# Performance work log

Measured on AMD Instinct MI355X. Metric: run time of the kernel, lower is better.

The kernel has to match this reference:

```python
import jax, jax.numpy as jnp
import numpy as np
from jax import lax

DIM = 256
NUM_HEADS = 8
HEAD_DIM = DIM // NUM_HEADS
DN = ('NCHW', 'OIHW', 'NCHW')


def _dsconv(x, dw, dwb, pw, pwb):
    # depthwise 3x3 (groups = C) then pointwise 1x1
    C = x.shape[1]
    y = lax.conv_general_dilated(x, dw, (1, 1), 'SAME',
                                 dimension_numbers=DN,
                                 feature_group_count=C)
    y = y + dwb[None, :, None, None]
    y = lax.conv_general_dilated(y, pw, (1, 1), 'SAME', dimension_numbers=DN)
    return y + pwb[None, :, None, None]


def _to_heads(x):
    # (B, C, H, W) -> (B, nh, HW, hd)
    B, C, H, W = x.shape
    return x.reshape(B, NUM_HEADS, HEAD_DIM, H * W).transpose(0, 1, 3, 2)


def setup_inputs() -> dict:
    key = jax.random.key(0)
    ks = jax.random.split(key, 14)
    B, H, W = 2, 64, 64
    inp = {
        'x': jax.random.normal(ks[0], (B, DIM, H, W), jnp.float32),
        'ctx': jax.random.normal(ks[1], (B, DIM, H, W), jnp.float32),
    }
    i = 2
    for name in ('q', 'k', 'v'):
        inp[f'{name}_dw'] = jax.random.normal(ks[i], (DIM, 1, 3, 3), jnp.float32) * 0.05; i += 1
        inp[f'{name}_dwb'] = jnp.zeros((DIM,), jnp.float32)
        inp[f'{name}_pw'] = jax.random.normal(ks[i], (DIM, DIM, 1, 1), jnp.float32) * 0.05; i += 1
        inp[f'{name}_pwb'] = jnp.zeros((DIM,), jnp.float32)
    return inp


def reference(x, ctx,
              q_dw, q_dwb, q_pw, q_pwb,
              k_dw, k_dwb, k_pw, k_pwb,
              v_dw, v_dwb, v_pw, v_pwb):
    B, C, H, W = x.shape
    scale = HEAD_DIM ** 0.5
    q = _to_heads(_dsconv(x, q_dw, q_dwb, q_pw, q_pwb))    # (B, nh, HW, hd)
    k = _to_heads(_dsconv(ctx, k_dw, k_dwb, k_pw, k_pwb))
    v = _to_heads(_dsconv(ctx, v_dw, v_dwb, v_pw, v_pwb))
    attn = jnp.einsum('bnqd,bnkd->bnqk', q, k) / scale      # (B, nh, HW, HW)
    attn = jax.nn.softmax(attn, axis=-1)
    out = jnp.einsum('bnqk,bnkd->bnqd', attn, v)            # (B, nh, HW, hd)
    out = out.transpose(0, 1, 3, 2).reshape(B, DIM, H * W)  # (B, dim, HW)
    return out
```

## Files before the change

### kernel.cpp

```cpp
#include <hip/hip_runtime.h>
#include <hip/hip_bf16.h>


#define HW 4096
#define CDIM 256
#define SCALE_LOG2E 0.2550348543f

typedef short bf16x8 __attribute__((ext_vector_type(8)));
typedef float f32x2 __attribute__((ext_vector_type(2)));
typedef float f32x4 __attribute__((ext_vector_type(4)));
typedef float f32x16 __attribute__((ext_vector_type(16)));

__device__ inline unsigned short f2bf(float f) {
  unsigned u = __float_as_uint(f);
  u = (u + 0x7fffu + ((u >> 16) & 1u)) >> 16;
  return (unsigned short)u;
}

__device__ inline unsigned cvtpk(float lo, float hi) {
  unsigned r;
  asm("v_cvt_pk_bf16_f32 %0, %1, %2" : "=v"(r) : "v"(lo), "v"(hi));
  return r;
}

__device__ inline float fexp2(float x) {
#if __has_builtin(__builtin_amdgcn_exp2f)
  return __builtin_amdgcn_exp2f(x);
#else
  return exp2f(x);
#endif
}

__device__ inline void plswap(unsigned& a, unsigned& b) {
#if __has_builtin(__builtin_amdgcn_permlane32_swap)
  auto r = __builtin_amdgcn_permlane32_swap((int)a, (int)b, false, false);
  a = (unsigned)r[0];
  b = (unsigned)r[1];
#else
  unsigned as = __shfl_xor((int)a, 32), bs = __shfl_xor((int)b, 32);
  bool hi = (threadIdx.x & 32) != 0;
  unsigned na = hi ? bs : a;
  unsigned nb = hi ? b : as;
  a = na; b = nb;
#endif
}

__global__ __launch_bounds__(256) void dw_all(
    const float* __restrict__ x, const float* __restrict__ ctx,
    const float* __restrict__ qdw, const float* __restrict__ qdwb,
    const float* __restrict__ kdw, const float* __restrict__ kdwb,
    const float* __restrict__ vdw, const float* __restrict__ vdwb,
    unsigned short* __restrict__ tq, unsigned short* __restrict__ tk,
    unsigned short* __restrict__ tv) {
  int gid = blockIdx.x * 256 + threadIdx.x;
  int pass = gid >> 19;
  int r = gid & 524287;
  int q4 = r & 1023;
  int plane = r >> 10;
  int c = plane & 255;
  int w0 = (q4 & 15) * 4, h = q4 >> 4;
  const float* src = (pass ? ctx : x) + (size_t)plane * HW;

  float e[3][6];
#pragma unroll
  for (int kh = 0; kh < 3; ++kh) {
    int hh = h + kh - 1;
    if (hh < 0 || hh > 63) {
#pragma unroll
      for (int j = 0; j < 6; ++j) e[kh][j] = 0.f;
    } else {
      const float* row = src + hh * 64 + w0;
      float4 m = *(const float4*)row;
      e[kh][0] = (w0 > 0) ? row[-1] : 0.f;
      e[kh][1] = m.x; e[kh][2] = m.y; e[kh][3] = m.z; e[kh][4] = m.w;
      e[kh][5] = (w0 < 60) ? row[4] : 0.f;
    }
  }
  size_t obase = (size_t)plane * HW + h * 64 + w0;
  if (pass == 0) {
    const float* wc = qdw + c * 9;
    float bv = qdwb[c];
    float a0 = bv, a1 = bv, a2 = bv, a3 = bv;
#pragma unroll
    for (int kh = 0; kh < 3; ++kh) {
      float w_0 = wc[kh * 3], w_1 = wc[kh * 3 + 1], w_2 = wc[kh * 3 + 2];
      a0 += w_0 * e[kh][0] + w_1 * e[kh][1] + w_2 * e[kh][2];
      a1 += w_0 * e[kh][1] + w_1 * e[kh][2] + w_2 * e[kh][3];
      a2 += w_0 * e[kh][2] + w_1 * e[kh][3] + w_2 * e[kh][4];
      a3 += w_0 * e[kh][3] + w_1 * e[kh][4] + w_2 * e[kh][5];
    }
    *(ushort4*)(tq + obase) = make_ushort4(f2bf(a0), f2bf(a1), f2bf(a2), f2bf(a3));
  } else {
    const float* wk = kdw + c * 9;
    const float* wvv = vdw + c * 9;
    float bk = kdwb[c], bv2 = vdwb[c];
    float k0 = bk, k1 = bk, k2 = bk, k3 = bk;
    float v0 = bv2, v1 = bv2, v2 = bv2, v3 = bv2;
#pragma unroll
    for (int kh = 0; kh < 3; ++kh) {
      float kw0 = wk[kh * 3], kw1 = wk[kh * 3 + 1], kw2 = wk[kh * 3 + 2];
      float vw0 = wvv[kh * 3], vw1 = wvv[kh * 3 + 1], vw2 = wvv[kh * 3 + 2];
      k0 += kw0 * e[kh][0] + kw1 * e[kh][1] + kw2 * e[kh][2];
      k1 += kw0 * e[kh][1] + kw1 * e[kh][2] + kw2 * e[kh][3];
      k2 += kw0 * e[kh][2] + kw1 * e[kh][3] + kw2 * e[kh][4];
      k3 += kw0 * e[kh][3] + kw1 * e[kh][4] + kw2 * e[kh][5];
      v0 += vw0 * e[kh][0] + vw1 * e[kh][1] + vw2 * e[kh][2];
      v1 += vw0 * e[kh][1] + vw1 * e[kh][2] + vw2 * e[kh][3];
      v2 += vw0 * e[kh][2] + vw1 * e[kh][3] + vw2 * e[kh][4];
      v3 += vw0 * e[kh][3] + vw1 * e[kh][4] + vw2 * e[kh][5];
    }
    *(ushort4*)(tk + obase) = make_ushort4(f2bf(k0), f2bf(k1), f2bf(k2), f2bf(k3));
    *(ushort4*)(tv + obase) = make_ushort4(f2bf(v0), f2bf(v1), f2bf(v2), f2bf(v3));
  }
}

__global__ __launch_bounds__(256) void pw_all(
    const unsigned short* __restrict__ tq, const unsigned short* __restrict__ tk,
    const unsigned short* __restrict__ tv,
    const float* __restrict__ qw, const float* __restrict__ qbs,
    const float* __restrict__ kw, const float* __restrict__ kbs,
    const float* __restrict__ vw, const float* __restrict__ vbs,
    unsigned short* __restrict__ Qc, unsigned short* __restrict__ Kc,
    unsigned short* __restrict__ Vc) {
  __shared__ __align__(16) unsigned char Bs[64 * 512];
  int tt = blockIdx.x >> 9;
  int bid = blockIdx.x & 511;
  const unsigned short* t = tt == 0 ? tq : (tt == 1 ? tk : tv);
  const float* w = tt == 0 ? qw : (tt == 1 ? kw : vw);
  const float* bias = tt == 0 ? qbs : (tt == 1 ? kbs : vbs);
  unsigned short* out = tt == 0 ? Qc : (tt == 1 ? Kc : Vc);
  float oscale = tt == 0 ? SCALE_LOG2E : 1.0f;

  int pt = bid & 63, cot = (bid >> 6) & 3, bb = bid >> 8;
  int p0 = pt * 64, co0 = cot * 64;
  int tid = threadIdx.x;
  int wv = tid >> 6, l = tid & 63, lq = l & 15, lg = l >> 4;

  bf16x8 af[8];
  {
    const float* wr = w + (size_t)(co0 + wv * 16 + lq) * 256;
#pragma unroll
    for (int kt = 0; kt < 8; ++kt) {
      float4 a = *(const float4*)(wr + kt * 32 + lg * 8);
      float4 bq = *(const float4*)(wr + kt * 32 + lg * 8 + 4);
      union { unsigned u[4]; bf16x8 v; } cv;
      cv.u[0] = cvtpk(a.x, a.y);  cv.u[1] = cvtpk(a.z, a.w);
      cv.u[2] = cvtpk(bq.x, bq.y); cv.u[3] = cvtpk(bq.z, bq.w);
      af[kt] = cv.v;
    }
  }
  {
    int cb = tid >> 3, po = tid & 7;
    const unsigned short* src = t + (size_t)bb * (CDIM * HW) + (size_t)(cb * 8) * HW + p0 + po * 8;
    uint4 r[8];
#pragma unroll
    for (int i = 0; i < 8; ++i) r[i] = *(const uint4*)(src + (size_t)i * HW);
#pragma unroll
    for (int jj = 0; jj < 8; ++jj) {
      uint4 o;
#pragma unroll
      for (int ww = 0; ww < 4; ++ww) {
        unsigned a = ((const unsigned*)&r[2 * ww])[jj >> 1];
        unsigned b = ((const unsigned*)&r[2 * ww + 1])[jj >> 1];
        unsigned lo = (jj & 1) ? (a >> 16) : (a & 0xffffu);
        unsigned hi = (jj & 1) ? (b & 0xffff0000u) : (b << 16);
        (&o.x)[ww] = lo | hi;
      }
      int p = po * 8 + jj;
      int swz = ((p ^ (p >> 3)) & 7) << 4;
      *(uint4*)(Bs + p * 512 + ((cb * 16) ^ swz)) = o;
    }
  }
  __syncthreads();
  f32x4 acc[4] = {};
#pragma unroll
  for (int nt = 0; nt < 4; ++nt) {
    int p = nt * 16 + lq;
    int swz = ((p ^ (p >> 3)) & 7) << 4;
    const unsigned char* Bp = Bs + p * 512;
#pragma unroll
    for (int kt = 0; kt < 8; ++kt) {
      bf16x8 bf = *(const bf16x8*)(Bp + ((kt * 64 + lg * 16) ^ swz));
      acc[nt] = __builtin_amdgcn_mfma_f32_16x16x32_bf16(af[kt], bf, acc[nt], 0, 0, 0);
    }
  }
  if (tt < 2) {
    int co = co0 + wv * 16 + lg * 4;
    int d0 = co & 31;
    float b0 = bias[co], b1 = bias[co + 1], b2 = bias[co + 2], b3 = bias[co + 3];
    size_t rowb = (size_t)(bb * 8 + (co >> 5)) * HW;
#pragma unroll
    for (int nt = 0; nt < 4; ++nt) {
      int p = p0 + nt * 16 + lq;
      ushort4 pk = make_ushort4(f2bf((acc[nt][0] + b0) * oscale),
                                f2bf((acc[nt][1] + b1) * oscale),
                                f2bf((acc[nt][2] + b2) * oscale),
                                f2bf((acc[nt][3] + b3) * oscale));
      *(ushort4*)(out + (rowb + p) * 32 + d0) = pk;
    }
  } else {
    int cob = co0 + wv * 16 + lg * 4;
#pragma unroll
    for (int r = 0; r < 4; ++r) {
      float bv = bias[cob + r];
      size_t rb = (size_t)bb * (CDIM * HW) + (size_t)(cob + r) * HW + p0;
#pragma unroll
      for (int nt = 0; nt < 4; ++nt)
        out[rb + nt * 16 + lq] = f2bf(acc[nt][r] + bv);
    }
  }
}

struct AttnState {
  bf16x8 qfh0, qfh1;
  f32x16 OA, OB, ZZ;
  float ps;
  int lq, hi;
};

__device__ inline void attn_compute(AttnState& S, const unsigned char* Kcur,
                                    const unsigned char* Vcur) {
#pragma unroll
  for (int t2 = 0; t2 < 2; ++t2) {
    const unsigned char* Krow = Kcur + (t2 * 32 + S.lq) * 80 + S.hi * 16;
    bf16x8 kfa = *(const bf16x8*)(Krow);
    bf16x8 kfb = *(const bf16x8*)(Krow + 32);
    __builtin_amdgcn_s_setprio(1);
    f32x16 st = __builtin_amdgcn_mfma_f32_32x32x16_bf16(kfa, S.qfh0, S.ZZ, 0, 0, 0);
    st = __builtin_amdgcn_mfma_f32_32x32x16_bf16(kfb, S.qfh1, st, 0, 0, 0);
    __builtin_amdgcn_s_setprio(0);
    float p[16];
#pragma unroll
    for (int r = 0; r < 16; ++r) p[r] = fexp2(st[r]);
    f32x2 a0 = {p[0], p[1]},  a1 = {p[2], p[3]};
    f32x2 a2 = {p[4], p[5]},  a3 = {p[6], p[7]};
    f32x2 a4 = {p[8], p[9]},  a5 = {p[10], p[11]};
    f32x2 a6 = {p[12], p[13]}, a7 = {p[14], p[15]};
    f32x2 b0 = a0 + a1, b1 = a2 + a3, b2 = a4 + a5, b3 = a6 + a7;
    f32x2 c0 = b0 + b1, c1 = b2 + b3;
    f32x2 d0 = c0 + c1;
    S.ps += d0[0] + d0[1];
    unsigned u0 = cvtpk(p[0], p[1]),  u1 = cvtpk(p[2], p[3]);
    unsigned u2 = cvtpk(p[4], p[5]),  u3 = cvtpk(p[6], p[7]);
    unsigned u4 = cvtpk(p[8], p[9]),  u5 = cvtpk(p[10], p[11]);
    unsigned u6 = cvtpk(p[12], p[13]), u7 = cvtpk(p[14], p[15]);
    plswap(u0, u2);
    plswap(u1, u3);
    plswap(u4, u6);
    plswap(u5, u7);
    union { unsigned w[4]; bf16x8 v; } A0, A1;
    A0.w[0] = u0; A0.w[1] = u1; A0.w[2] = u2; A0.w[3] = u3;
    A1.w[0] = u4; A1.w[1] = u5; A1.w[2] = u6; A1.w[3] = u7;
    const unsigned char* Vrow = Vcur + S.lq * 144 + t2 * 64;
    bf16x8 vf0 = *(const bf16x8*)(Vrow + S.hi * 16);
    bf16x8 vf1 = *(const bf16x8*)(Vrow + 32 + S.hi * 16);
    __builtin_amdgcn_s_setprio(1);
    S.OA = __builtin_amdgcn_mfma_f32_32x32x16_bf16(A0.v, vf0, S.OA, 0, 0, 0);
    S.OB = __builtin_amdgcn_mfma_f32_32x32x16_bf16(A1.v, vf1, S.OB, 0, 0, 0);
    __builtin_amdgcn_s_setprio(0);
  }
}

__global__ __launch_bounds__(512, 4) void attn_kernel(
    const unsigned short* __restrict__ Qt, const unsigned short* __restrict__ Kt,
    const unsigned short* __restrict__ Vn, float* __restrict__ out) {
  __shared__ __align__(16) unsigned char lds[38912];
  int bid0 = blockIdx.x;
  int bid = (bid0 & 7) * 64 + (bid0 >> 3);
  int qb = bid & 31, bh = bid >> 5;
  int b = bh >> 3, n = bh & 7;
  int tid = threadIdx.x;
  int l = tid & 63, wv = tid >> 6;
  int qg = wv & 3, ks = wv >> 2;

  AttnState S;
  S.lq = l & 31; S.hi = l >> 5;
  S.OA = (f32x16){}; S.OB = (f32x16){}; S.ZZ = (f32x16){};
  S.ps = 0.f;

  const unsigned short* Qg = Qt + (size_t)bh * (HW * 32);
  const unsigned short* Kg = Kt + (size_t)bh * (HW * 32);
  const unsigned short* Vg = Vn + (size_t)(b * CDIM + n * 32) * HW;

  int q0 = qb * 128 + qg * 32;
  S.qfh0 = *(const bf16x8*)(Qg + (size_t)(q0 + S.lq) * 32 + S.hi * 8);
  S.qfh1 = *(const bf16x8*)(Qg + (size_t)(q0 + S.lq) * 32 + 16 + S.hi * 8);

  int ht = tid & 255;
  int krow = ht >> 2, kcol = ht & 3;
  int vrow = ht >> 3, vcol = ht & 7;
  unsigned char* Kb0 = lds + (ks * 2 + 0) * 5120;
  unsigned char* Kb1 = lds + (ks * 2 + 1) * 5120;
  unsigned char* Vb0 = lds + 20480 + (ks * 2 + 0) * 4608;
  unsigned char* Vb1 = lds + 20480 + (ks * 2 + 1) * 4608;
  unsigned char* Kw0 = Kb0 + krow * 80 + kcol * 16;
  unsigned char* Kw1 = Kb1 + krow * 80 + kcol * 16;
  unsigned char* Vw0 = Vb0 + vrow * 144 + vcol * 16;
  unsigned char* Vw1 = Vb1 + vrow * 144 + vcol * 16;
  const uint4* Ksrc = (const uint4*)(Kg + (size_t)(ks * 2048) * 32);
  const unsigned short* Vsrc = Vg + (size_t)vrow * HW + ks * 2048 + vcol * 8;

  uint4 kst = Ksrc[krow * 4 + kcol];
  uint4 vst = *(const uint4*)Vsrc;
  *(uint4*)Kw0 = kst;
  *(uint4*)Vw0 = vst;
  kst = Ksrc[(64 + krow) * 4 + kcol];
  vst = *(const uint4*)(Vsrc + 64);

#pragma unroll 1
  for (int c = 0; c < 32; c += 2) {
    __syncthreads();
    *(uint4*)Kw1 = kst;
    *(uint4*)Vw1 = vst;
    if (c < 30) {
      kst = Ksrc[((c + 2) * 64 + krow) * 4 + kcol];
      vst = *(const uint4*)(Vsrc + (c + 2) * 64);
    }
    attn_compute(S, Kb0, Vb0);
    __syncthreads();
    if (c < 30) {
      *(uint4*)Kw0 = kst;
      *(uint4*)Vw0 = vst;
      kst = Ksrc[((c + 3) * 64 + krow) * 4 + kcol];
      vst = *(const uint4*)(Vsrc + (c + 3) * 64);
    }
    attn_compute(S, Kb1, Vb1);
  }

  f32x16 O = S.OA + S.OB;
  float ps = S.ps;
  int lq = S.lq, hi = S.hi;
  ps += __shfl_xor(ps, 32);
  __syncthreads();
  float* Ox = (float*)lds;
  float* SumX = (float*)(lds + 16896);
  if (ks == 1) {
    float* Or = Ox + qg * (32 * 33) + lq * 33;
#pragma unroll
    for (int rr = 0; rr < 4; ++rr) {
      float4 vv = {O[rr * 4 + 0], O[rr * 4 + 1], O[rr * 4 + 2], O[rr * 4 + 3]};
      *(float4*)(Or + 8 * rr + 4 * hi) = vv;
    }
    if (hi == 0) SumX[qg * 32 + lq] = ps;
  }
  __syncthreads();
  if (ks == 0) {
    const float* Or = Ox + qg * (32 * 33) + lq * 33;
    float rtot = ps + SumX[qg * 32 + lq];
    float rv = 1.0f / rtot;
    size_t ob = ((size_t)(b * CDIM) + n * 32 + lq) * HW;
#pragma unroll
    for (int rr = 0; rr < 4; ++rr) {
      int qlb = 8 * rr + 4 * hi;
      float4 part = *(const float4*)(Or + qlb);
      float4 res;
#pragma unroll
      for (int j = 0; j < 4; ++j) {
        float sq = __int_as_float(
            __builtin_amdgcn_ds_bpermute((qlb + j) * 4, __float_as_int(rv)));
        (&res.x)[j] = (O[rr * 4 + j] + (&part.x)[j]) * sq;
      }
      *(float4*)(out + ob + q0 + qlb) = res;
    }
  }
}

extern "C" void kernel_launch(void* const* d_in, const int* in_sizes, int n_in,
                              void* d_out, int out_size, void* d_ws, size_t ws_size,
                              hipStream_t stream) {
  const float* x   = (const float*)d_in[0];
  const float* ctx = (const float*)d_in[1];
  const float* q_dw  = (const float*)d_in[2];
  const float* q_dwb = (const float*)d_in[3];
  const float* q_pw  = (const float*)d_in[4];
  const float* q_pwb = (const float*)d_in[5];
  const float* k_dw  = (const float*)d_in[6];
  const float* k_dwb = (const float*)d_in[7];
  const float* k_pw  = (const float*)d_in[8];
  const float* k_pwb = (const float*)d_in[9];
  const float* v_dw  = (const float*)d_in[10];
  const float* v_dwb = (const float*)d_in[11];
  const float* v_pw  = (const float*)d_in[12];
  const float* v_pwb = (const float*)d_in[13];

  const size_t N = (size_t)2 * CDIM * HW;
  unsigned short* Qc = (unsigned short*)d_ws;
  unsigned short* Kc = Qc + N;
  unsigned short* Vc = Kc + N;
  unsigned short* tv = Vc + N;
  unsigned short* tq = (unsigned short*)d_out;
  unsigned short* tk = tq + N;

  dw_all<<<4096, 256, 0, stream>>>(x, ctx, q_dw, q_dwb, k_dw, k_dwb, v_dw, v_dwb,
                                   tq, tk, tv);
  pw_all<<<1536, 256, 0, stream>>>(tq, tk, tv, q_pw, q_pwb, k_pw, k_pwb,
                                   v_pw, v_pwb, Qc, Kc, Vc);
  attn_kernel<<<512, 512, 0, stream>>>(Qc, Kc, Vc, (float*)d_out);
}
```

Measured before the change: 85.61 us.

## Process two query tiles per wave and split keys four ways in 1024-thread blocks

Each wave now holds two 32-row query tiles and reuses every K/V fragment read from LDS for both, which halves LDS fragment traffic per unit of work. Blocks grow to 1024 threads with four key splits, so there are 256 blocks of 256 queries each. A multi-stage LDS reduction merges the four partial outputs and row sums. The cost is higher register pressure, a larger LDS footprint that limits resident blocks, and fewer blocks than CUs, which may leave some hardware idle.

Result: slower. 141.2 us (+64.9%).

```diff
diff --git a/kernel.cpp b/kernel.cpp
--- a/kernel.cpp
+++ b/kernel.cpp
@@ -211,156 +211,221 @@
   }
 }
 
-struct AttnState {
-  bf16x8 qfh0, qfh1;
-  f32x16 OA, OB, ZZ;
-  float ps;
+
+__device__ inline void softmax_tile(const f32x16& st, float& ps, bf16x8& A0v, bf16x8& A1v) {
+  float p[16];
+#pragma unroll
+  for (int r = 0; r < 16; ++r) p[r] = fexp2(st[r]);
+  f32x2 a0 = {p[0], p[1]},  a1 = {p[2], p[3]};
+  f32x2 a2 = {p[4], p[5]},  a3 = {p[6], p[7]};
+  f32x2 a4 = {p[8], p[9]},  a5 = {p[10], p[11]};
+  f32x2 a6 = {p[12], p[13]}, a7 = {p[14], p[15]};
+  f32x2 b0 = a0 + a1, b1 = a2 + a3, b2 = a4 + a5, b3 = a6 + a7;
+  f32x2 c0 = b0 + b1, c1 = b2 + b3;
+  f32x2 d0 = c0 + c1;
+  ps += d0[0] + d0[1];
+  unsigned u0 = cvtpk(p[0], p[1]),  u1 = cvtpk(p[2], p[3]);
+  unsigned u2 = cvtpk(p[4], p[5]),  u3 = cvtpk(p[6], p[7]);
+  unsigned u4 = cvtpk(p[8], p[9]),  u5 = cvtpk(p[10], p[11]);
+  unsigned u6 = cvtpk(p[12], p[13]), u7 = cvtpk(p[14], p[15]);
+  plswap(u0, u2);
+  plswap(u1, u3);
+  plswap(u4, u6);
+  plswap(u5, u7);
+  union { unsigned w[4]; bf16x8 v; } A0, A1;
+  A0.w[0] = u0; A0.w[1] = u1; A0.w[2] = u2; A0.w[3] = u3;
+  A1.w[0] = u4; A1.w[1] = u5; A1.w[2] = u6; A1.w[3] = u7;
+  A0v = A0.v; A1v = A1.v;
+}
+
+struct AState {
+  bf16x8 qa0, qa1, qb0, qb1;
+  f32x16 Oa, Ob, ZZ;
+  float psa, psb;
   int lq, hi;
 };
 
-__device__ inline void attn_compute(AttnState& S, const unsigned char* Kcur,
-                                    const unsigned char* Vcur) {
+__device__ inline void attn_compute(AState& S, const unsigned char* Kb,
+                                    const unsigned char* Vb) {
 #pragma unroll
   for (int t2 = 0; t2 < 2; ++t2) {
-    const unsigned char* Krow = Kcur + (t2 * 32 + S.lq) * 80 + S.hi * 16;
+    const unsigned char* Krow = Kb + (t2 * 32 + S.lq) * 80 + S.hi * 16;
     bf16x8 kfa = *(const bf16x8*)(Krow);
     bf16x8 kfb = *(const bf16x8*)(Krow + 32);
-    __builtin_amdgcn_s_setprio(1);
-    f32x16 st = __builtin_amdgcn_mfma_f32_32x32x16_bf16(kfa, S.qfh0, S.ZZ, 0, 0, 0);
-    st = __builtin_amdgcn_mfma_f32_32x32x16_bf16(kfb, S.qfh1, st, 0, 0, 0);
-    __builtin_amdgcn_s_setprio(0);
-    float p[16];
-#pragma unroll
-    for (int r = 0; r < 16; ++r) p[r] = fexp2(st[r]);
-    f32x2 a0 = {p[0], p[1]},  a1 = {p[2], p[3]};
-    f32x2 a2 = {p[4], p[5]},  a3 = {p[6], p[7]};
-    f32x2 a4 = {p[8], p[9]},  a5 = {p[10], p[11]};
-    f32x2 a6 = {p[12], p[13]}, a7 = {p[14], p[15]};
-    f32x2 b0 = a0 + a1, b1 = a2 + a3, b2 = a4 + a5, b3 = a6 + a7;
-    f32x2 c0 = b0 + b1, c1 = b2 + b3;
-    f32x2 d0 = c0 + c1;
-    S.ps += d0[0] + d0[1];
-    unsigned u0 = cvtpk(p[0], p[1]),  u1 = cvtpk(p[2], p[3]);
-    unsigned u2 = cvtpk(p[4], p[5]),  u3 = cvtpk(p[6], p[7]);
-    unsigned u4 = cvtpk(p[8], p[9]),  u5 = cvtpk(p[10], p[11]);
-    unsigned u6 = cvtpk(p[12], p[13]), u7 = cvtpk(p[14], p[15]);
-    plswap(u0, u2);
-    plswap(u1, u3);
-    plswap(u4, u6);
-    plswap(u5, u7);
-    union { unsigned w[4]; bf16x8 v; } A0, A1;
-    A0.w[0] = u0; A0.w[1] = u1; A0.w[2] = u2; A0.w[3] = u3;
-    A1.w[0] = u4; A1.w[1] = u5; A1.w[2] = u6; A1.w[3] = u7;
-    const unsigned char* Vrow = Vcur + S.lq * 144 + t2 * 64;
+    const unsigned char* Vrow = Vb + S.lq * 176 + t2 * 64;
     bf16x8 vf0 = *(const bf16x8*)(Vrow + S.hi * 16);
     bf16x8 vf1 = *(const bf16x8*)(Vrow + 32 + S.hi * 16);
     __builtin_amdgcn_s_setprio(1);
-    S.OA = __builtin_amdgcn_mfma_f32_32x32x16_bf16(A0.v, vf0, S.OA, 0, 0, 0);
-    S.OB = __builtin_amdgcn_mfma_f32_32x32x16_bf16(A1.v, vf1, S.OB, 0, 0, 0);
+    f32x16 st = __builtin_amdgcn_mfma_f32_32x32x16_bf16(kfa, S.qa0, S.ZZ, 0, 0, 0);
+    st = __builtin_amdgcn_mfma_f32_32x32x16_bf16(kfb, S.qa1, st, 0, 0, 0);
     __builtin_amdgcn_s_setprio(0);
-  }
-}
-
-__global__ __launch_bounds__(512, 4) void attn_kernel(
+    bf16x8 A0, A1;
+    softmax_tile(st, S.psa, A0, A1);
+    __builtin_amdgcn_s_setprio(1);
+    S.Oa = __builtin_amdgcn_mfma_f32_32x32x16_bf16(A0, vf0, S.Oa, 0, 0, 0);
+    S.Oa = __builtin_amdgcn_mfma_f32_32x32x16_bf16(A1, vf1, S.Oa, 0, 0, 0);
+    st = __builtin_amdgcn_mfma_f32_32x32x16_bf16(kfa, S.qb0, S.ZZ, 0, 0, 0);
+    st = __builtin_amdgcn_mfma_f32_32x32x16_bf16(kfb, S.qb1, st, 0, 0, 0);
+    __builtin_amdgcn_s_setprio(0);
+    softmax_tile(st, S.psb, A0, A1);
+    __builtin_amdgcn_s_setprio(1);
+    S.Ob = __builtin_amdgcn_mfma_f32_32x32x16_bf16(A0, vf0, S.Ob, 0, 0, 0);
+    S.Ob = __builtin_amdgcn_mfma_f32_32x32x16_bf16(A1, vf1, S.Ob, 0, 0, 0);
+    __builtin_amdgcn_s_setprio(0);
+  }
+}
+
+__global__ __launch_bounds__(1024, 4) void attn_kernel(
     const unsigned short* __restrict__ Qt, const unsigned short* __restrict__ Kt,
     const unsigned short* __restrict__ Vn, float* __restrict__ out) {
-  __shared__ __align__(16) unsigned char lds[38912];
+  __shared__ __align__(16) unsigned char lds[86016];
   int bid0 = blockIdx.x;
-  int bid = (bid0 & 7) * 64 + (bid0 >> 3);
-  int qb = bid & 31, bh = bid >> 5;
+  int bid = (bid0 & 7) * 32 + (bid0 >> 3);
+  int qb = bid & 15, bh = bid >> 4;
   int b = bh >> 3, n = bh & 7;
   int tid = threadIdx.x;
   int l = tid & 63, wv = tid >> 6;
   int qg = wv & 3, ks = wv >> 2;
 
-  AttnState S;
+  AState S;
   S.lq = l & 31; S.hi = l >> 5;
-  S.OA = (f32x16){}; S.OB = (f32x16){}; S.ZZ = (f32x16){};
-  S.ps = 0.f;
+  S.Oa = (f32x16){}; S.Ob = (f32x16){}; S.ZZ = (f32x16){};
+  S.psa = 0.f; S.psb = 0.f;
 
   const unsigned short* Qg = Qt + (size_t)bh * (HW * 32);
   const unsigned short* Kg = Kt + (size_t)bh * (HW * 32);
   const unsigned short* Vg = Vn + (size_t)(b * CDIM + n * 32) * HW;
 
-  int q0 = qb * 128 + qg * 32;
-  S.qfh0 = *(const bf16x8*)(Qg + (size_t)(q0 + S.lq) * 32 + S.hi * 8);
-  S.qfh1 = *(const bf16x8*)(Qg + (size_t)(q0 + S.lq) * 32 + 16 + S.hi * 8);
-
-  int ht = tid & 255;
-  int krow = ht >> 2, kcol = ht & 3;
-  int vrow = ht >> 3, vcol = ht & 7;
-  unsigned char* Kb0 = lds + (ks * 2 + 0) * 5120;
-  unsigned char* Kb1 = lds + (ks * 2 + 1) * 5120;
-  unsigned char* Vb0 = lds + 20480 + (ks * 2 + 0) * 4608;
-  unsigned char* Vb1 = lds + 20480 + (ks * 2 + 1) * 4608;
-  unsigned char* Kw0 = Kb0 + krow * 80 + kcol * 16;
-  unsigned char* Kw1 = Kb1 + krow * 80 + kcol * 16;
-  unsigned char* Vw0 = Vb0 + vrow * 144 + vcol * 16;
-  unsigned char* Vw1 = Vb1 + vrow * 144 + vcol * 16;
-  const uint4* Ksrc = (const uint4*)(Kg + (size_t)(ks * 2048) * 32);
-  const unsigned short* Vsrc = Vg + (size_t)vrow * HW + ks * 2048 + vcol * 8;
-
-  uint4 kst = Ksrc[krow * 4 + kcol];
-  uint4 vst = *(const uint4*)Vsrc;
+  int q0 = qb * 256 + qg * 64;
+  S.qa0 = *(const bf16x8*)(Qg + (size_t)(q0 + S.lq) * 32 + S.hi * 8);
+  S.qa1 = *(const bf16x8*)(Qg + (size_t)(q0 + S.lq) * 32 + 16 + S.hi * 8);
+  S.qb0 = *(const bf16x8*)(Qg + (size_t)(q0 + 32 + S.lq) * 32 + S.hi * 8);
+  S.qb1 = *(const bf16x8*)(Qg + (size_t)(q0 + 32 + S.lq) * 32 + 16 + S.hi * 8);
+
+  int sk = tid >> 8, r = tid & 255;
+  int krow = r >> 2, kcol = r & 3;
+  int vrow = r >> 3, vcol = r & 7;
+  unsigned char* Kp0 = lds + sk * 10240;
+  unsigned char* Vp0 = lds + 40960 + sk * 11264;
+  unsigned char* Kw0 = Kp0 + krow * 80 + kcol * 16;
+  unsigned char* Kw1 = Kw0 + 5120;
+  unsigned char* Vw0 = Vp0 + vrow * 176 + vcol * 16;
+  unsigned char* Vw1 = Vw0 + 5632;
+  const uint4* Ksrc4 = (const uint4*)(Kg + (size_t)(sk * 1024) * 32);
+  const unsigned short* Vsrcp = Vg + (size_t)vrow * HW + sk * 1024 + vcol * 8;
+
+  const unsigned char* Kb0 = lds + ks * 10240;
+  const unsigned char* Kb1 = Kb0 + 5120;
+  const unsigned char* Vb0 = lds + 40960 + ks * 11264;
+  const unsigned char* Vb1 = Vb0 + 5632;
+
+  uint4 kst = Ksrc4[krow * 4 + kcol];
+  uint4 vst = *(const uint4*)Vsrcp;
   *(uint4*)Kw0 = kst;
   *(uint4*)Vw0 = vst;
-  kst = Ksrc[(64 + krow) * 4 + kcol];
-  vst = *(const uint4*)(Vsrc + 64);
+  kst = Ksrc4[(64 + krow) * 4 + kcol];
+  vst = *(const uint4*)(Vsrcp + 64);
 
 #pragma unroll 1
-  for (int c = 0; c < 32; c += 2) {
+  for (int c = 0; c < 16; c += 2) {
     __syncthreads();
     *(uint4*)Kw1 = kst;
     *(uint4*)Vw1 = vst;
-    if (c < 30) {
-      kst = Ksrc[((c + 2) * 64 + krow) * 4 + kcol];
-      vst = *(const uint4*)(Vsrc + (c + 2) * 64);
+    if (c < 14) {
+      kst = Ksrc4[((c + 2) * 64 + krow) * 4 + kcol];
+      vst = *(const uint4*)(Vsrcp + (c + 2) * 64);
     }
     attn_compute(S, Kb0, Vb0);
     __syncthreads();
-    if (c < 30) {
+    if (c < 14) {
       *(uint4*)Kw0 = kst;
       *(uint4*)Vw0 = vst;
-      kst = Ksrc[((c + 3) * 64 + krow) * 4 + kcol];
-      vst = *(const uint4*)(Vsrc + (c + 3) * 64);
+      kst = Ksrc4[((c + 3) * 64 + krow) * 4 + kcol];
+      vst = *(const uint4*)(Vsrcp + (c + 3) * 64);
     }
     attn_compute(S, Kb1, Vb1);
   }
 
-  f32x16 O = S.OA + S.OB;
-  float ps = S.ps;
+  float psa = S.psa + __shfl_xor(S.psa, 32);
+  float psb = S.psb + __shfl_xor(S.psb, 32);
   int lq = S.lq, hi = S.hi;
-  ps += __shfl_xor(ps, 32);
   __syncthreads();
-  float* Ox = (float*)lds;
-  float* SumX = (float*)(lds + 16896);
-  if (ks == 1) {
-    float* Or = Ox + qg * (32 * 33) + lq * 33;
-#pragma unroll
-    for (int rr = 0; rr < 4; ++rr) {
-      float4 vv = {O[rr * 4 + 0], O[rr * 4 + 1], O[rr * 4 + 2], O[rr * 4 + 3]};
-      *(float4*)(Or + 8 * rr + 4 * hi) = vv;
-    }
-    if (hi == 0) SumX[qg * 32 + lq] = ps;
+  float* MO = (float*)lds;
+  float* MS = (float*)(lds + 67584);
+  float* moq = MO + qg * (64 * 33);
+  float* msq = MS + qg * 64;
+  const int setStride = 4 * 64 * 33;
+
+  if (ks == 1 || ks == 3) {
+    int set = (ks == 3);
+    float* base = moq + set * setStride;
+#pragma unroll
+    for (int r2 = 0; r2 < 16; ++r2) {
+      int qr = (r2 & 3) + 8 * (r2 >> 2) + 4 * hi;
+      base[qr * 33 + lq] = S.Oa[r2];
+      base[(32 + qr) * 33 + lq] = S.Ob[r2];
+    }
+    if (hi == 0) {
+      msq[set * 256 + lq] = psa;
+      msq[set * 256 + 32 + lq] = psb;
+    }
+  }
+  __syncthreads();
+  if (ks == 0 || ks == 2) {
+    int set = (ks == 2);
+    const float* base = moq + set * setStride;
+#pragma unroll
+    for (int r2 = 0; r2 < 16; ++r2) {
+      int qr = (r2 & 3) + 8 * (r2 >> 2) + 4 * hi;
+      S.Oa[r2] += base[qr * 33 + lq];
+      S.Ob[r2] += base[(32 + qr) * 33 + lq];
+    }
+    psa += msq[set * 256 + lq];
+    psb += msq[set * 256 + 32 + lq];
+  }
+  __syncthreads();
+  if (ks == 2) {
+    float* base = moq;
+#pragma unroll
+    for (int r2 = 0; r2 < 16; ++r2) {
+      int qr = (r2 & 3) + 8 * (r2 >> 2) + 4 * hi;
+      base[qr * 33 + lq] = S.Oa[r2];
+      base[(32 + qr) * 33 + lq] = S.Ob[r2];
+    }
+    if (hi == 0) {
+      msq[lq] = psa;
+      msq[32 + lq] = psb;
+    }
   }
   __syncthreads();
   if (ks == 0) {
-    const float* Or = Ox + qg * (32 * 33) + lq * 33;
-    float rtot = ps + SumX[qg * 32 + lq];
-    float rv = 1.0f / rtot;
+    const float* base = moq;
+#pragma unroll
+    for (int r2 = 0; r2 < 16; ++r2) {
+      int qr = (r2 & 3) + 8 * (r2 >> 2) + 4 * hi;
+      S.Oa[r2] += base[qr * 33 + lq];
+      S.Ob[r2] += base[(32 + qr) * 33 + lq];
+    }
+    psa += msq[lq];
+    psb += msq[32 + lq];
+    float rva = 1.0f / psa;
+    float rvb = 1.0f / psb;
     size_t ob = ((size_t)(b * CDIM) + n * 32 + lq) * HW;
 #pragma unroll
     for (int rr = 0; rr < 4; ++rr) {
       int qlb = 8 * rr + 4 * hi;
-      float4 part = *(const float4*)(Or + qlb);
-      float4 res;
+      float4 ra, rb;
 #pragma unroll
       for (int j = 0; j < 4; ++j) {
-        float sq = __int_as_float(
-            __builtin_amdgcn_ds_bpermute((qlb + j) * 4, __float_as_int(rv)));
-        (&res.x)[j] = (O[rr * 4 + j] + (&part.x)[j]) * sq;
+        float sa = __int_as_float(
+            __builtin_amdgcn_ds_bpermute((qlb + j) * 4, __float_as_int(rva)));
+        float sb = __int_as_float(
+            __builtin_amdgcn_ds_bpermute((qlb + j) * 4, __float_as_int(rvb)));
+        (&ra.x)[j] = S.Oa[rr * 4 + j] * sa;
+        (&rb.x)[j] = S.Ob[rr * 4 + j] * sb;
       }
-      *(float4*)(out + ob + q0 + qlb) = res;
+      *(float4*)(out + ob + q0 + qlb) = ra;
+      *(float4*)(out + ob + q0 + 32 + qlb) = rb;
     }
   }
 }
@@ -395,5 +460,5 @@
                                    tq, tk, tv);
   pw_all<<<1536, 256, 0, stream>>>(tq, tk, tv, q_pw, q_pwb, k_pw, k_pwb,
                                    v_pw, v_pwb, Qc, Kc, Vc);
-  attn_kernel<<<512, 512, 0, stream>>>(Qc, Kc, Vc, (float*)d_out);
-}
+  attn_kernel<<<256, 1024, 0, stream>>>(Qc, Kc, Vc, (float*)d_out);
+}
```

## Restructure attention into 4-wave split-KV blocks with wave-private LDS and 64-query reuse

Applied to the files above, without the earlier changes.

The attention kernel moves from 512-thread blocks to 256-thread blocks. Each block now has four waves, and each wave covers its own quarter of the keys for 64 queries, processed as two 32-query subtiles that share the same K/V fragments. Each wave stages its K/V chunk into a private LDS region, prefetched through registers, so the main loop has no block-wide barriers. The four partial outputs and row sums are combined at the end with a two-level LDS reduction, and the output is written in transposed d-major form. The aim is to remove the per-chunk __syncthreads, get more query reuse per K/V load, and raise occupancy. In exchange the final merge costs more and the single LDS buffer leaves less room to hide load latency.

Measured after the change: 87.65 us. 2.4% more time.

```diff
diff --git a/kernel.cpp b/kernel.cpp
--- a/kernel.cpp
+++ b/kernel.cpp
@@ -211,35 +211,65 @@
   }
 }
 
-struct AttnState {
-  bf16x8 qfh0, qfh1;
-  f32x16 OA, OB, ZZ;
-  float ps;
-  int lq, hi;
-};
-
-__device__ inline void attn_compute(AttnState& S, const unsigned char* Kcur,
-                                    const unsigned char* Vcur) {
-#pragma unroll
-  for (int t2 = 0; t2 < 2; ++t2) {
-    const unsigned char* Krow = Kcur + (t2 * 32 + S.lq) * 80 + S.hi * 16;
-    bf16x8 kfa = *(const bf16x8*)(Krow);
-    bf16x8 kfb = *(const bf16x8*)(Krow + 32);
+__global__ __launch_bounds__(256, 3) void attn_kernel(
+    const unsigned short* __restrict__ Qt, const unsigned short* __restrict__ Kt,
+    const unsigned short* __restrict__ Vn, float* __restrict__ out) {
+  __shared__ __align__(16) unsigned char lds[20480];
+  int bid0 = blockIdx.x;
+  int bid = (bid0 & 7) * 128 + (bid0 >> 3);
+  int qb = bid & 63, bh = bid >> 6;
+  int b = bh >> 3, n = bh & 7;
+  int tid = threadIdx.x;
+  int l = tid & 63, ks = tid >> 6;
+  int lq = l & 31, hi = l >> 5;
+
+  const unsigned short* Qg = Qt + (size_t)bh * (HW * 32);
+  const unsigned short* Kg = Kt + (size_t)bh * (HW * 32);
+  const unsigned short* Vg = Vn + (size_t)(b * CDIM + n * 32) * HW;
+
+  int q0 = qb * 64;
+  bf16x8 qa0 = *(const bf16x8*)(Qg + (size_t)(q0 + lq) * 32 + hi * 8);
+  bf16x8 qa1 = *(const bf16x8*)(Qg + (size_t)(q0 + lq) * 32 + 16 + hi * 8);
+  bf16x8 qB0 = *(const bf16x8*)(Qg + (size_t)(q0 + 32 + lq) * 32 + hi * 8);
+  bf16x8 qB1 = *(const bf16x8*)(Qg + (size_t)(q0 + 32 + lq) * 32 + 16 + hi * 8);
+
+  f32x16 Oa = {}, Ob = {}, ZZ = {};
+  float psa = 0.f, psb = 0.f;
+
+  unsigned char* Kl = lds + ks * 5120;
+  unsigned char* Vl = Kl + 2560;
+  int u0i = l, u1i = l + 64;
+  unsigned char* Kw0 = Kl + (u0i >> 2) * 80 + (u0i & 3) * 16;
+  unsigned char* Kw1 = Kl + (u1i >> 2) * 80 + (u1i & 3) * 16;
+  unsigned char* Vw0 = Vl + (u0i >> 2) * 80 + (u0i & 3) * 16;
+  unsigned char* Vw1 = Vl + (u1i >> 2) * 80 + (u1i & 3) * 16;
+  const uint4* Ks4 = (const uint4*)Kg + (size_t)ks * 4096;
+  const unsigned short* Vs0 = Vg + (size_t)(u0i >> 2) * HW + ks * 1024 + (u0i & 3) * 8;
+  const unsigned short* Vs1 = Vg + (size_t)(u1i >> 2) * HW + ks * 1024 + (u1i & 3) * 8;
+
+  uint4 ks0 = Ks4[u0i], ks1 = Ks4[u1i];
+  uint4 vs0 = *(const uint4*)Vs0, vs1 = *(const uint4*)Vs1;
+  *(uint4*)Kw0 = ks0; *(uint4*)Kw1 = ks1;
+  *(uint4*)Vw0 = vs0; *(uint4*)Vw1 = vs1;
+
+  const unsigned char* Kr = Kl + lq * 80 + hi * 16;
+  const unsigned char* Vr = Vl + lq * 80 + hi * 16;
+
+  auto subtile = [&](bf16x8 kfa, bf16x8 kfb, bf16x8 va, bf16x8 vb,
+                     bf16x8 qf0, bf16x8 qf1, f32x16& O, float& ps) {
     __builtin_amdgcn_s_setprio(1);
-    f32x16 st = __builtin_amdgcn_mfma_f32_32x32x16_bf16(kfa, S.qfh0, S.ZZ, 0, 0, 0);
-    st = __builtin_amdgcn_mfma_f32_32x32x16_bf16(kfb, S.qfh1, st, 0, 0, 0);
+    f32x16 st = __builtin_amdgcn_mfma_f32_32x32x16_bf16(kfa, qf0, ZZ, 0, 0, 0);
+    st = __builtin_amdgcn_mfma_f32_32x32x16_bf16(kfb, qf1, st, 0, 0, 0);
     __builtin_amdgcn_s_setprio(0);
     float p[16];
 #pragma unroll
     for (int r = 0; r < 16; ++r) p[r] = fexp2(st[r]);
-    f32x2 a0 = {p[0], p[1]},  a1 = {p[2], p[3]};
-    f32x2 a2 = {p[4], p[5]},  a3 = {p[6], p[7]};
-    f32x2 a4 = {p[8], p[9]},  a5 = {p[10], p[11]};
-    f32x2 a6 = {p[12], p[13]}, a7 = {p[14], p[15]};
-    f32x2 b0 = a0 + a1, b1 = a2 + a3, b2 = a4 + a5, b3 = a6 + a7;
-    f32x2 c0 = b0 + b1, c1 = b2 + b3;
-    f32x2 d0 = c0 + c1;
-    S.ps += d0[0] + d0[1];
+    f32x2 s0 = (f32x2){p[0], p[1]} + (f32x2){p[2], p[3]};
+    f32x2 s1 = (f32x2){p[4], p[5]} + (f32x2){p[6], p[7]};
+    f32x2 s2 = (f32x2){p[8], p[9]} + (f32x2){p[10], p[11]};
+    f32x2 s3 = (f32x2){p[12], p[13]} + (f32x2){p[14], p[15]};
+    f32x2 s4 = (s0 + s1) + (s2 + s3);
+    ps += s4[0] + s4[1];
     unsigned u0 = cvtpk(p[0], p[1]),  u1 = cvtpk(p[2], p[3]);
     unsigned u2 = cvtpk(p[4], p[5]),  u3 = cvtpk(p[6], p[7]);
     unsigned u4 = cvtpk(p[8], p[9]),  u5 = cvtpk(p[10], p[11]);
@@ -248,119 +278,99 @@
     plswap(u1, u3);
     plswap(u4, u6);
     plswap(u5, u7);
-    union { unsigned w[4]; bf16x8 v; } A0, A1;
-    A0.w[0] = u0; A0.w[1] = u1; A0.w[2] = u2; A0.w[3] = u3;
-    A1.w[0] = u4; A1.w[1] = u5; A1.w[2] = u6; A1.w[3] = u7;
-    const unsigned char* Vrow = Vcur + S.lq * 144 + t2 * 64;
-    bf16x8 vf0 = *(const bf16x8*)(Vrow + S.hi * 16);
-    bf16x8 vf1 = *(const bf16x8*)(Vrow + 32 + S.hi * 16);
+    union { unsigned w[4]; bf16x8 v; } X1, X2;
+    X1.w[0] = u0; X1.w[1] = u1; X1.w[2] = u2; X1.w[3] = u3;
+    X2.w[0] = u4; X2.w[1] = u5; X2.w[2] = u6; X2.w[3] = u7;
     __builtin_amdgcn_s_setprio(1);
-    S.OA = __builtin_amdgcn_mfma_f32_32x32x16_bf16(A0.v, vf0, S.OA, 0, 0, 0);
-    S.OB = __builtin_amdgcn_mfma_f32_32x32x16_bf16(A1.v, vf1, S.OB, 0, 0, 0);
+    O = __builtin_amdgcn_mfma_f32_32x32x16_bf16(va, X1.v, O, 0, 0, 0);
+    O = __builtin_amdgcn_mfma_f32_32x32x16_bf16(vb, X2.v, O, 0, 0, 0);
     __builtin_amdgcn_s_setprio(0);
-  }
-}
-
-__global__ __launch_bounds__(512, 4) void attn_kernel(
-    const unsigned short* __restrict__ Qt, const unsigned short* __restrict__ Kt,
-    const unsigned short* __restrict__ Vn, float* __restrict__ out) {
-  __shared__ __align__(16) unsigned char lds[38912];
-  int bid0 = blockIdx.x;
-  int bid = (bid0 & 7) * 64 + (bid0 >> 3);
-  int qb = bid & 31, bh = bid >> 5;
-  int b = bh >> 3, n = bh & 7;
-  int tid = threadIdx.x;
-  int l = tid & 63, wv = tid >> 6;
-  int qg = wv & 3, ks = wv >> 2;
-
-  AttnState S;
-  S.lq = l & 31; S.hi = l >> 5;
-  S.OA = (f32x16){}; S.OB = (f32x16){}; S.ZZ = (f32x16){};
-  S.ps = 0.f;
-
-  const unsigned short* Qg = Qt + (size_t)bh * (HW * 32);
-  const unsigned short* Kg = Kt + (size_t)bh * (HW * 32);
-  const unsigned short* Vg = Vn + (size_t)(b * CDIM + n * 32) * HW;
-
-  int q0 = qb * 128 + qg * 32;
-  S.qfh0 = *(const bf16x8*)(Qg + (size_t)(q0 + S.lq) * 32 + S.hi * 8);
-  S.qfh1 = *(const bf16x8*)(Qg + (size_t)(q0 + S.lq) * 32 + 16 + S.hi * 8);
-
-  int ht = tid & 255;
-  int krow = ht >> 2, kcol = ht & 3;
-  int vrow = ht >> 3, vcol = ht & 7;
-  unsigned char* Kb0 = lds + (ks * 2 + 0) * 5120;
-  unsigned char* Kb1 = lds + (ks * 2 + 1) * 5120;
-  unsigned char* Vb0 = lds + 20480 + (ks * 2 + 0) * 4608;
-  unsigned char* Vb1 = lds + 20480 + (ks * 2 + 1) * 4608;
-  unsigned char* Kw0 = Kb0 + krow * 80 + kcol * 16;
-  unsigned char* Kw1 = Kb1 + krow * 80 + kcol * 16;
-  unsigned char* Vw0 = Vb0 + vrow * 144 + vcol * 16;
-  unsigned char* Vw1 = Vb1 + vrow * 144 + vcol * 16;
-  const uint4* Ksrc = (const uint4*)(Kg + (size_t)(ks * 2048) * 32);
-  const unsigned short* Vsrc = Vg + (size_t)vrow * HW + ks * 2048 + vcol * 8;
-
-  uint4 kst = Ksrc[krow * 4 + kcol];
-  uint4 vst = *(const uint4*)Vsrc;
-  *(uint4*)Kw0 = kst;
-  *(uint4*)Vw0 = vst;
-  kst = Ksrc[(64 + krow) * 4 + kcol];
-  vst = *(const uint4*)(Vsrc + 64);
+  };
 
 #pragma unroll 1
-  for (int c = 0; c < 32; c += 2) {
-    __syncthreads();
-    *(uint4*)Kw1 = kst;
-    *(uint4*)Vw1 = vst;
-    if (c < 30) {
-      kst = Ksrc[((c + 2) * 64 + krow) * 4 + kcol];
-      vst = *(const uint4*)(Vsrc + (c + 2) * 64);
-    }
-    attn_compute(S, Kb0, Vb0);
-    __syncthreads();
-    if (c < 30) {
-      *(uint4*)Kw0 = kst;
-      *(uint4*)Vw0 = vst;
-      kst = Ksrc[((c + 3) * 64 + krow) * 4 + kcol];
-      vst = *(const uint4*)(Vsrc + (c + 3) * 64);
-    }
-    attn_compute(S, Kb1, Vb1);
-  }
-
-  f32x16 O = S.OA + S.OB;
-  float ps = S.ps;
-  int lq = S.lq, hi = S.hi;
-  ps += __shfl_xor(ps, 32);
+  for (int c = 0; c < 32; ++c) {
+    bf16x8 kfa = *(const bf16x8*)(Kr);
+    bf16x8 kfb = *(const bf16x8*)(Kr + 32);
+    bf16x8 va  = *(const bf16x8*)(Vr);
+    bf16x8 vb  = *(const bf16x8*)(Vr + 32);
+    if (c < 31) {
+      ks0 = Ks4[(c + 1) * 128 + u0i];
+      ks1 = Ks4[(c + 1) * 128 + u1i];
+      vs0 = *(const uint4*)(Vs0 + (c + 1) * 32);
+      vs1 = *(const uint4*)(Vs1 + (c + 1) * 32);
+    }
+    subtile(kfa, kfb, va, vb, qa0, qa1, Oa, psa);
+    subtile(kfa, kfb, va, vb, qB0, qB1, Ob, psb);
+    if (c < 31) {
+      *(uint4*)Kw0 = ks0; *(uint4*)Kw1 = ks1;
+      *(uint4*)Vw0 = vs0; *(uint4*)Vw1 = vs1;
+    }
+  }
+
+  psa += __shfl_xor(psa, 32);
+  psb += __shfl_xor(psb, 32);
   __syncthreads();
-  float* Ox = (float*)lds;
-  float* SumX = (float*)(lds + 16896);
-  if (ks == 1) {
-    float* Or = Ox + qg * (32 * 33) + lq * 33;
-#pragma unroll
-    for (int rr = 0; rr < 4; ++rr) {
-      float4 vv = {O[rr * 4 + 0], O[rr * 4 + 1], O[rr * 4 + 2], O[rr * 4 + 3]};
-      *(float4*)(Or + 8 * rr + 4 * hi) = vv;
-    }
-    if (hi == 0) SumX[qg * 32 + lq] = ps;
+  float* MO = (float*)lds;
+  float* MS = (float*)lds + 4224;
+  const int SET = 2112, SUB = 1056;
+
+  if (ks == 1 || ks == 3) {
+    int s = (ks == 3);
+#pragma unroll
+    for (int r = 0; r < 16; ++r) {
+      int d = (r & 3) + 8 * (r >> 2) + 4 * hi;
+      MO[s * SET + d * 33 + lq] = Oa[r];
+      MO[s * SET + SUB + d * 33 + lq] = Ob[r];
+    }
+    if (hi == 0) {
+      MS[s * 128 + lq] = psa;
+      MS[s * 128 + 32 + lq] = psb;
+    }
+  }
+  __syncthreads();
+  if (ks == 0 || ks == 2) {
+    int s = (ks == 2);
+#pragma unroll
+    for (int r = 0; r < 16; ++r) {
+      int d = (r & 3) + 8 * (r >> 2) + 4 * hi;
+      Oa[r] += MO[s * SET + d * 33 + lq];
+      Ob[r] += MO[s * SET + SUB + d * 33 + lq];
+    }
+    psa += MS[s * 128 + lq];
+    psb += MS[s * 128 + 32 + lq];
+  }
+  __syncthreads();
+  if (ks == 2) {
+#pragma unroll
+    for (int r = 0; r < 16; ++r) {
+      int d = (r & 3) + 8 * (r >> 2) + 4 * hi;
+      MO[d * 33 + lq] = Oa[r];
+      MO[SUB + d * 33 + lq] = Ob[r];
+    }
+    if (hi == 0) {
+      MS[lq] = psa;
+      MS[32 + lq] = psb;
+    }
   }
   __syncthreads();
   if (ks == 0) {
-    const float* Or = Ox + qg * (32 * 33) + lq * 33;
-    float rtot = ps + SumX[qg * 32 + lq];
-    float rv = 1.0f / rtot;
-    size_t ob = ((size_t)(b * CDIM) + n * 32 + lq) * HW;
-#pragma unroll
-    for (int rr = 0; rr < 4; ++rr) {
-      int qlb = 8 * rr + 4 * hi;
-      float4 part = *(const float4*)(Or + qlb);
-      float4 res;
-#pragma unroll
-      for (int j = 0; j < 4; ++j) {
-        float sq = __int_as_float(
-            __builtin_amdgcn_ds_bpermute((qlb + j) * 4, __float_as_int(rv)));
-        (&res.x)[j] = (O[rr * 4 + j] + (&part.x)[j]) * sq;
+    float rva, rvb;
+    {
+#pragma unroll
+      for (int r = 0; r < 16; ++r) {
+        int d = (r & 3) + 8 * (r >> 2) + 4 * hi;
+        Oa[r] += MO[d * 33 + lq];
+        Ob[r] += MO[SUB + d * 33 + lq];
       }
-      *(float4*)(out + ob + q0 + qlb) = res;
+      rva = 1.0f / (psa + MS[lq]);
+      rvb = 1.0f / (psb + MS[32 + lq]);
+    }
+    size_t ob = ((size_t)(b * CDIM) + n * 32) * HW;
+#pragma unroll
+    for (int r = 0; r < 16; ++r) {
+      int d = (r & 3) + 8 * (r >> 2) + 4 * hi;
+      out[ob + (size_t)d * HW + q0 + lq] = Oa[r] * rva;
+      out[ob + (size_t)d * HW + q0 + 32 + lq] = Ob[r] * rvb;
     }
   }
 }
@@ -395,5 +405,5 @@
                                    tq, tk, tv);
   pw_all<<<1536, 256, 0, stream>>>(tq, tk, tv, q_pw, q_pwb, k_pw, k_pwb,
                                    v_pw, v_pwb, Qc, Kc, Vc);
-  attn_kernel<<<512, 512, 0, stream>>>(Qc, Kc, Vc, (float*)d_out);
-}
+  attn_kernel<<<1024, 256, 0, stream>>>(Qc, Kc, Vc, (float*)d_out);
+}
```
